# Performance work log

Measured on AMD Instinct MI355X. Metric: run time of the kernel, lower is better.

Reference implementation:

```python
import jax, jax.numpy as jnp
import numpy as np

# dims
B, L, DM, DS, K, E, DFF, R = 16, 1024, 512, 16, 4, 2, 2048, 32
DI = DM  # expand = 1 -> d_inner == d_model

PARAM_NAMES = ['m_in_w','m_conv_w','m_conv_b','m_xproj_w','m_dt_w','m_dt_b','m_A_log','m_D','m_out_w']


def setup_inputs() -> dict:
    key = jax.random.key(0)
    ks = iter(jax.random.split(key, 32))
    def rn(shape, scale=0.02):
        return jax.random.normal(next(ks), shape, dtype=jnp.float32) * scale
    inp = {
        'x': jax.random.normal(next(ks), (B, L, DM), dtype=jnp.float32),
        # per layer (E) and per direction (2: forward mamba, reversed mamba)
        'm_in_w':   rn((E, 2, 2 * DI, DM)),
        'm_conv_w': rn((E, 2, DI, K), 0.1),
        'm_conv_b': jnp.zeros((E, 2, DI), jnp.float32),
        'm_xproj_w': rn((E, 2, R + 2 * DS, DI)),
        'm_dt_w':   rn((E, 2, DI, R), 0.1),
        'm_dt_b':   jnp.full((E, 2, DI), -4.0, jnp.float32) + rn((E, 2, DI), 0.1),
        'm_A_log':  jnp.log(jnp.broadcast_to(jnp.arange(1, DS + 1, dtype=jnp.float32), (E, 2, DI, DS))),
        'm_D':      jnp.ones((E, 2, DI), jnp.float32),
        'm_out_w':  rn((E, 2, DM, DI)),
        # FFN (1x1 convs == linears) and norms per layer
        'ff_w1': rn((E, DFF, DM)), 'ff_b1': jnp.zeros((E, DFF), jnp.float32),
        'ff_w2': rn((E, DM, DFF)), 'ff_b2': jnp.zeros((E, DM), jnp.float32),
        'ln1_g': jnp.ones((E, DM), jnp.float32), 'ln1_b': jnp.zeros((E, DM), jnp.float32),
        'ln2_g': jnp.ones((E, DM), jnp.float32), 'ln2_b': jnp.zeros((E, DM), jnp.float32),
        'lnf_g': jnp.ones((DM,), jnp.float32),   'lnf_b': jnp.zeros((DM,), jnp.float32),
    }
    return inp


def layer_norm(x, g, b, eps=1e-5):
    mu = x.mean(-1, keepdims=True)
    var = ((x - mu) ** 2).mean(-1, keepdims=True)
    return (x - mu) * jax.lax.rsqrt(var + eps) * g + b


def mamba(x, in_w, conv_w, conv_b, xproj_w, dt_w, dt_b, A_log, Dp, out_w):
    # x: (B, L, DM)
    Bsz, Lseq, _ = x.shape
    xz = x @ in_w.T                       # (B, L, 2*DI)
    xc, z = jnp.split(xz, 2, axis=-1)
    # depthwise causal conv1d (kernel K, left pad K-1, truncate to L)
    xp = jnp.pad(xc, ((0, 0), (K - 1, 0), (0, 0)))
    xc = sum(conv_w[:, k] * xp[:, k:k + Lseq, :] for k in range(K)) + conv_b
    xc = jax.nn.silu(xc)
    dbl = xc @ xproj_w.T                  # (B, L, R + 2*DS)
    dt, Bm, Cm = dbl[..., :R], dbl[..., R:R + DS], dbl[..., R + DS:]
    dt = jax.nn.softplus(dt @ dt_w.T + dt_b)  # (B, L, DI)
    A = -jnp.exp(A_log)                   # (DI, DS)

    def step(h, inputs):
        dt_t, B_t, C_t, x_t = inputs      # (B,DI) (B,DS) (B,DS) (B,DI)
        dA = jnp.exp(dt_t[..., None] * A)             # (B, DI, DS)
        h = dA * h + (dt_t * x_t)[..., None] * B_t[:, None, :]
        y = jnp.einsum('bds,bs->bd', h, C_t)
        return h, y

    xs = (dt.transpose(1, 0, 2), Bm.transpose(1, 0, 2), Cm.transpose(1, 0, 2), xc.transpose(1, 0, 2))
    h0 = jnp.zeros((Bsz, DI, DS), dtype=x.dtype)
    _, ys = jax.lax.scan(step, h0, xs)    # ys: (L, B, DI)
    y = ys.transpose(1, 0, 2) + xc * Dp
    y = y * jax.nn.silu(z)
    return y @ out_w.T                    # (B, L, DM)


def _forward(x, m_in_w, m_conv_w, m_conv_b, m_xproj_w, m_dt_w, m_dt_b, m_A_log, m_D, m_out_w,
             ff_w1, ff_b1, ff_w2, ff_b2, ln1_g, ln1_b, ln2_g, ln2_b, lnf_g, lnf_b):
    packs = (m_in_w, m_conv_w, m_conv_b, m_xproj_w, m_dt_w, m_dt_b, m_A_log, m_D, m_out_w)
    for e in range(E):
        p_fwd = tuple(a[e, 0] for a in packs)
        p_rev = tuple(a[e, 1] for a in packs)
        # bidirectional mamba mixing (second block sees the time-flipped sequence)
        new_x = mamba(x, *p_fwd) + mamba(x[:, ::-1], *p_rev)[:, ::-1]
        x = x + new_x
        xn = layer_norm(x, ln1_g[e], ln1_b[e])
        y = jax.nn.gelu(xn @ ff_w1[e].T + ff_b1[e], approximate=False)
        y = y @ ff_w2[e].T + ff_b2[e]
        x = layer_norm(xn + y, ln2_g[e], ln2_b[e])
    return layer_norm(x, lnf_g, lnf_b)


def reference(x, m_in_w, m_conv_w, m_conv_b, m_xproj_w, m_dt_w, m_dt_b, m_A_log, m_D, m_out_w,
              ff_w1, ff_b1, ff_w2, ff_b2, ln1_g, ln1_b, ln2_g, ln2_b, lnf_g, lnf_b):
    return _forward(x, m_in_w, m_conv_w, m_conv_b, m_xproj_w, m_dt_w, m_dt_b, m_A_log, m_D, m_out_w,
                    ff_w1, ff_b1, ff_w2, ff_b2, ln1_g, ln1_b, ln2_g, ln2_b, lnf_g, lnf_b)
```

## Files before the change

kernel.cpp:

```cpp
#include <hip/hip_runtime.h>
#include <hip/hip_bf16.h>
#include <math.h>

#define DEVI __device__ __forceinline__

namespace {
constexpr int kL   = 1024;
constexpr int kDM  = 512;
constexpr int kDS  = 16;
constexpr int kDFF = 2048;
constexpr int kR   = 32;
constexpr int kDI  = 512;
constexpr int kB   = 16;
constexpr int kM   = kB * kL;
constexpr int kNC  = 16;
constexpr int kCH  = kL / kNC;
constexpr float kLOG2E = 1.4426950408889634f;
}

typedef __attribute__((ext_vector_type(8))) short short8;
typedef __attribute__((ext_vector_type(4))) float f32x4;

DEVI float silu_f(float x)     { return x / (1.f + __expf(-x)); }
DEVI float softplus_f(float x) { return fmaxf(x, 0.f) + log1pf(__expf(-fabsf(x))); }
DEVI float gelu_f(float x)     { return 0.5f * x * (1.f + erff(x * 0.70710678118654752f)); }

DEVI float fexp2(float x) {
    float r;
    asm("v_exp_f32 %0, %1" : "=v"(r) : "v"(x));
    return r;
}

DEVI unsigned short f2bf(float f) {
    unsigned int u = __float_as_uint(f);
    return (unsigned short)((u + 0x7fffu + ((u >> 16) & 1u)) >> 16);
}
DEVI float bf2f(unsigned short u) {
    return __uint_as_float(((unsigned int)u) << 16);
}
DEVI uint2 pack4(float4 v) {
    uint2 p;
    p.x = (unsigned int)f2bf(v.x) | ((unsigned int)f2bf(v.y) << 16);
    p.y = (unsigned int)f2bf(v.z) | ((unsigned int)f2bf(v.w) << 16);
    return p;
}

DEVI void powtree16(float r, float* qq) {
    qq[0] = r;
#pragma unroll
    for (int s = 1; s < 16; ++s) {
        int a = (s - 1) >> 1, b = (s - 1) - a;
        qq[s] = qq[a] * qq[b];
    }
}

typedef const __attribute__((address_space(1))) unsigned int* gas1;
typedef __attribute__((address_space(3))) unsigned int* las3;
DEVI void gload16(const unsigned short* g, unsigned short* l) {
    __builtin_amdgcn_global_load_lds((gas1)g, (las3)l, 16, 0, 0);
}

struct WCvtArgs { const float* src[6]; unsigned int end[6]; };

__global__ __launch_bounds__(256) void cvt_weights_k(
    WCvtArgs a, unsigned short* __restrict__ dst)
{
    unsigned int i = (blockIdx.x * 256 + threadIdx.x) * 4;
    if (i >= a.end[5]) return;
    int j = 0;
    while (i >= a.end[j]) ++j;
    unsigned int base = j ? a.end[j - 1] : 0;
    float4 v = *(const float4*)&a.src[j][i - base];
    *(uint2*)&dst[i] = pack4(v);
}

__global__ __launch_bounds__(256) void init_x_k(
    const float* __restrict__ x, float* __restrict__ xo,
    unsigned short* __restrict__ xb)
{
    size_t i = (size_t)(blockIdx.x * 256 + threadIdx.x) * 4;
    float4 v = *(const float4*)&x[i];
    *(float4*)&xo[i] = v;
    *(uint2*)&xb[i] = pack4(v);
}

template <int EPI, int BN, typename CT>
__global__ __launch_bounds__(256) void gemm_bf16(
    const unsigned short* __restrict__ A, int lda, size_t zA,
    const unsigned short* __restrict__ W, size_t zW,
    CT* __restrict__ C, int ldc, size_t zC,
    const float* __restrict__ biasb, int zBias,
    const unsigned short* __restrict__ add,
    unsigned short* __restrict__ auxb, size_t zAux, int Kd)
{
    static_assert(BN == 64 || BN == 128, "");
    constexpr int NF = BN / 32;
    __shared__ alignas(16) unsigned short As[2][128 * 32];
    __shared__ alignas(16) unsigned short Ws[2][BN * 32];

    const int z = blockIdx.z;
    A += (size_t)z * zA; W += (size_t)z * zW; C += (size_t)z * zC;
    const float* bias = biasb ? biasb + (size_t)z * zBias : nullptr;
    unsigned short* aux = auxb ? auxb + (size_t)z * zAux : nullptr;

    const int gx = gridDim.x;
    int flat = blockIdx.y * gx + blockIdx.x;
    const int total = gx * gridDim.y;
    if ((total & 7) == 0) {
        int q = total >> 3;
        flat = (flat & 7) * q + (flat >> 3);
    }
    const int bx = flat % gx;
    const int by = flat / gx;

    const int tid  = threadIdx.x;
    const int lane = tid & 63;
    const int wv   = tid >> 6;
    const int wm   = wv >> 1;
    const int wn   = wv & 1;
    const int row0 = by * 128;
    const int col0 = bx * BN;

    f32x4 acc[4][NF];
#pragma unroll
    for (int m = 0; m < 4; ++m)
#pragma unroll
        for (int n = 0; n < NF; ++n) acc[m][n] = (f32x4){0.f, 0.f, 0.f, 0.f};

    const int sr  = tid >> 2;
    const int scw = (((tid & 3) ^ ((tid >> 3) & 3)) * 8);
    const unsigned short* Ag = A + (size_t)(row0 + sr) * lda + scw;
    const unsigned short* Wg = W + (size_t)(col0 + sr) * Kd + scw;

    auto stage = [&](int buf, int k0) {
        gload16(Ag + k0, &As[buf][tid * 8]);
        gload16(Ag + (size_t)64 * lda + k0, &As[buf][2048 + tid * 8]);
        gload16(Wg + k0, &Ws[buf][tid * 8]);
        if (BN == 128)
            gload16(Wg + (size_t)64 * Kd + k0, &Ws[buf][2048 + tid * 8]);
    };

    const int nt = Kd / 32;
    stage(0, 0);
    if (nt > 1) stage(1, 32);

    const int fr  = lane & 15;
    const int sw8 = (((lane >> 4) ^ ((fr >> 1) & 3)) * 8);

    for (int t = 0; t < nt; ++t) {
        const int cur = t & 1;
        if (t + 1 < nt) {
            if constexpr (BN == 128) asm volatile("s_waitcnt vmcnt(4)" ::: "memory");
            else                     asm volatile("s_waitcnt vmcnt(3)" ::: "memory");
        } else {
            asm volatile("s_waitcnt vmcnt(0)" ::: "memory");
        }
        __builtin_amdgcn_sched_barrier(0);
        __builtin_amdgcn_s_barrier();
        __builtin_amdgcn_sched_barrier(0);

        short8 af[4], bf[NF];
#pragma unroll
        for (int m = 0; m < 4; ++m)
            af[m] = *(const short8*)&As[cur][(wm * 64 + m * 16 + fr) * 32 + sw8];
#pragma unroll
        for (int n = 0; n < NF; ++n)
            bf[n] = *(const short8*)&Ws[cur][(wn * (BN / 2) + n * 16 + fr) * 32 + sw8];
        __builtin_amdgcn_s_setprio(1);
#pragma unroll
        for (int m = 0; m < 4; ++m)
#pragma unroll
            for (int n = 0; n < NF; ++n)
                acc[m][n] = __builtin_amdgcn_mfma_f32_16x16x32_bf16(
                    af[m], bf[n], acc[m][n], 0, 0, 0);
        __builtin_amdgcn_s_setprio(0);

        __builtin_amdgcn_sched_barrier(0);
        __builtin_amdgcn_s_barrier();
        __builtin_amdgcn_sched_barrier(0);
        if (t + 2 < nt) stage(cur, (t + 2) * 32);
    }

    const int cr = (lane >> 4) * 4;
#pragma unroll
    for (int m = 0; m < 4; ++m) {
#pragma unroll
        for (int n = 0; n < NF; ++n) {
            int cn = col0 + wn * (BN / 2) + n * 16 + fr;
#pragma unroll
            for (int r = 0; r < 4; ++r) {
                int rr = row0 + wm * 64 + m * 16 + cr + r;
                size_t idx = (size_t)rr * ldc + cn;
                float v = acc[m][n][r];
                if constexpr (EPI == 0) {
                    if constexpr (__is_same(CT, unsigned short)) C[idx] = f2bf(v);
                    else C[idx] = v;
                } else if constexpr (EPI == 1) {
                    float sp = softplus_f(v + bias[cn]);
                    if constexpr (__is_same(CT, unsigned short)) C[idx] = f2bf(sp);
                    else C[idx] = sp;
                } else if constexpr (EPI == 3) {
                    C[idx] = f2bf(gelu_f(v + bias[cn]));
                } else if constexpr (EPI == 4) {
                    C[idx] = v + bias[cn] + bf2f(add[idx]);
                } else {
                    C[idx] = v;
                    if (cn < 32) aux[(size_t)rr * 32 + cn] = f2bf(v);
                }
            }
        }
    }
}

__global__ __launch_bounds__(128) void conv_silu_k(
    const unsigned short* __restrict__ xz2, unsigned short* __restrict__ xcb,
    const float* __restrict__ wb, const float* __restrict__ biasb)
{
    const int task = blockIdx.x * 128 + threadIdx.x;
    const int g   = task & 63;
    const int c   = (task >> 6) & 31;
    const int b   = (task >> 11) & 15;
    const int dir = (task >> 15) & 1;
    const int d0  = g * 8;

    const unsigned short* xzd = xz2 + (size_t)dir * 1024 + (size_t)b * kL * 2048 + d0;
    unsigned short* xc = xcb + (size_t)dir * kM * kDI + (size_t)b * kL * kDI + d0;
    const float* w    = wb + (size_t)dir * 2048;
    const float* bias = biasb + (size_t)dir * 512;

    float wk[4][8];
#pragma unroll
    for (int k = 0; k < 4; ++k)
#pragma unroll
        for (int j = 0; j < 8; ++j)
            wk[k][j] = w[(d0 + j) * 4 + (dir ? 3 - k : k)];
    float bs[8];
#pragma unroll
    for (int j = 0; j < 8; ++j) bs[j] = bias[d0 + j];

    const int t0 = c * 32;
    const int rbase = dir ? t0 : t0 - 3;

    auto loadrow = [&](int t, float* o) {
        if (t < 0 || t >= kL) {
#pragma unroll
            for (int j = 0; j < 8; ++j) o[j] = 0.f;
            return;
        }
        uint4 p = *(const uint4*)&xzd[(size_t)t * 2048];
        o[0] = bf2f((unsigned short)(p.x & 0xffff));
        o[1] = bf2f((unsigned short)(p.x >> 16));
        o[2] = bf2f((unsigned short)(p.y & 0xffff));
        o[3] = bf2f((unsigned short)(p.y >> 16));
        o[4] = bf2f((unsigned short)(p.z & 0xffff));
        o[5] = bf2f((unsigned short)(p.z >> 16));
        o[6] = bf2f((unsigned short)(p.w & 0xffff));
        o[7] = bf2f((unsigned short)(p.w >> 16));
    };

    float x0[8], x1[8], x2[8];
    loadrow(rbase + 0, x0);
    loadrow(rbase + 1, x1);
    loadrow(rbase + 2, x2);

#pragma unroll 4
    for (int i = 0; i < 32; ++i) {
        float x3[8];
        loadrow(rbase + 3 + i, x3);
        unsigned short o[8];
#pragma unroll
        for (int j = 0; j < 8; ++j) {
            float v = bs[j];
            v = fmaf(wk[0][j], x0[j], v);
            v = fmaf(wk[1][j], x1[j], v);
            v = fmaf(wk[2][j], x2[j], v);
            v = fmaf(wk[3][j], x3[j], v);
            o[j] = f2bf(silu_f(v));
        }
        *(uint4*)&xc[(size_t)(t0 + i) * kDI] = *(uint4*)o;
#pragma unroll
        for (int j = 0; j < 8; ++j) { x0[j] = x1[j]; x1[j] = x2[j]; x2[j] = x3[j]; }
    }
}

__global__ __launch_bounds__(256) void scan_chunk(
    const unsigned short* __restrict__ dtb2, const unsigned short* __restrict__ xcb2,
    const float* __restrict__ dbl2, const float* __restrict__ A_logb,
    float* __restrict__ S2, float* __restrict__ sdt2)
{
    int dir = blockIdx.y;
    const unsigned short* dtb = dtb2 + (size_t)dir * kM * kDI;
    const unsigned short* xcb = xcb2 + (size_t)dir * kM * kDI;
    const float* dbl = dbl2 + (size_t)dir * kM * 64;
    const float* A_log = A_logb + (size_t)dir * 8192;
    float* S   = S2 + (size_t)dir * (kB * kNC * kDS * kDI);
    float* sdt = sdt2 + (size_t)dir * (kB * kNC * kDI);

    int blk  = blockIdx.x;
    int dblk = blk & 1;
    int c    = (blk >> 1) & (kNC - 1);
    int b    = blk >> 5;
    int d    = dblk * 256 + threadIdx.x;

    __shared__ float blds[kCH][16];
    {
        int i = threadIdx.x >> 2, q = (threadIdx.x & 3) * 4;
        int t = dir ? (kL - 1 - (c * kCH + i)) : (c * kCH + i);
        *(float4*)&blds[i][q] =
            *(const float4*)&dbl[(size_t)(b * kL + t) * 64 + kR + q];
    }
    __syncthreads();

    const float* al = A_log + d * kDS;
    float A2[16];
#pragma unroll
    for (int s = 0; s < 16; ++s) A2[s] = -__expf(al[s]) * kLOG2E;

    bool fast = true;
#pragma unroll
    for (int s = 1; s < 16; ++s)
        fast = fast && (fabsf(A2[s] - A2[0] * (float)(s + 1)) <= 1e-4f * fabsf(A2[s]));

    float h[16];
#pragma unroll
    for (int s = 0; s < 16; ++s) h[s] = 0.f;
    float sum = 0.f;

    if (fast) {
        const float A0 = A2[0];
#pragma unroll 2
        for (int i = 0; i < kCH; ++i) {
            int p   = c * kCH + i;
            int t   = dir ? (kL - 1 - p) : p;
            int row = b * kL + t;
            float dt = bf2f(dtb[(size_t)row * kDI + d]);
            float xv = bf2f(xcb[(size_t)row * kDI + d]);
            sum += dt;
            float dx = dt * xv;
            float qq[16];
            powtree16(fexp2(dt * A0), qq);
            const float4* bp = (const float4*)&blds[i][0];
            float4 b0 = bp[0], b1 = bp[1], b2 = bp[2], b3 = bp[3];
            float Bv[16] = {b0.x, b0.y, b0.z, b0.w, b1.x, b1.y, b1.z, b1.w,
                            b2.x, b2.y, b2.z, b2.w, b3.x, b3.y, b3.z, b3.w};
#pragma unroll
            for (int s = 0; s < 16; ++s)
                h[s] = fmaf(qq[s], h[s], dx * Bv[s]);
        }
    } else {
#pragma unroll 2
        for (int i = 0; i < kCH; ++i) {
            int p   = c * kCH + i;
            int t   = dir ? (kL - 1 - p) : p;
            int row = b * kL + t;
            float dt = bf2f(dtb[(size_t)row * kDI + d]);
            float xv = bf2f(xcb[(size_t)row * kDI + d]);
            sum += dt;
            float dx = dt * xv;
            const float4* bp = (const float4*)&blds[i][0];
            float4 b0 = bp[0], b1 = bp[1], b2 = bp[2], b3 = bp[3];
            float Bv[16] = {b0.x, b0.y, b0.z, b0.w, b1.x, b1.y, b1.z, b1.w,
                            b2.x, b2.y, b2.z, b2.w, b3.x, b3.y, b3.z, b3.w};
#pragma unroll
            for (int s = 0; s < 16; ++s) {
                float q = fexp2(dt * A2[s]);
                h[s] = fmaf(q, h[s], dx * Bv[s]);
            }
        }
    }
    size_t base = (size_t)(b * kNC + c) * kDS * kDI + d;
#pragma unroll
    for (int s = 0; s < 16; ++s) S[base + s * kDI] = h[s];
    sdt[(size_t)(b * kNC + c) * kDI + d] = sum;
}

__global__ __launch_bounds__(256) void scan_carry(
    float* __restrict__ S2, const float* __restrict__ sdt2,
    const float* __restrict__ A_logb)
{
    int dir = blockIdx.y;
    float* S = S2 + (size_t)dir * (kB * kNC * kDS * kDI);
    const float* sdt = sdt2 + (size_t)dir * (kB * kNC * kDI);
    const float* A_log = A_logb + (size_t)dir * 8192;

    int g = blockIdx.x * 256 + threadIdx.x;
    int d = g & (kDI - 1);
    int s = (g >> 9) & 15;
    int b = g >> 13;

    float A2 = -__expf(A_log[d * kDS + s]) * kLOG2E;
    float h = 0.f;
#pragma unroll
    for (int c = 0; c < kNC; ++c) {
        size_t base = ((size_t)(b * kNC + c) * kDS + s) * kDI + d;
        float sv = S[base];
        float sd = sdt[(size_t)(b * kNC + c) * kDI + d];
        S[base] = h;
        h = fmaf(fexp2(sd * A2), h, sv);
    }
}

__global__ __launch_bounds__(256) void scan_emit(
    const unsigned short* __restrict__ dtb2, const unsigned short* __restrict__ xcb2,
    const float* __restrict__ dbl2, const float* __restrict__ A_logb,
    const float* __restrict__ h0v2, const float* __restrict__ Dpb,
    const unsigned short* __restrict__ xz2, unsigned short* __restrict__ yb2)
{
    int dir = blockIdx.y;
    const unsigned short* dtb = dtb2 + (size_t)dir * kM * kDI;
    const unsigned short* xcb = xcb2 + (size_t)dir * kM * kDI;
    const float* dbl = dbl2 + (size_t)dir * kM * 64;
    const float* A_log = A_logb + (size_t)dir * 8192;
    const float* h0v = h0v2 + (size_t)dir * (kB * kNC * kDS * kDI);
    const float* Dp = Dpb + (size_t)dir * 512;
    const unsigned short* zg = xz2 + (size_t)dir * 1024 + 512;
    unsigned short* yb = yb2 + (size_t)dir * kM * kDI;

    int blk  = blockIdx.x;
    int dblk = blk & 1;
    int c    = (blk >> 1) & (kNC - 1);
    int b    = blk >> 5;
    int d    = dblk * 256 + threadIdx.x;

    __shared__ float bclds[kCH][32];
    {
        int i0 = threadIdx.x >> 3, q = (threadIdx.x & 7) * 4;
#pragma unroll
        for (int rr = 0; rr < 2; ++rr) {
            int i = i0 + rr * 32;
            int t = dir ? (kL - 1 - (c * kCH + i)) : (c * kCH + i);
            *(float4*)&bclds[i][q] =
                *(const float4*)&dbl[(size_t)(b * kL + t) * 64 + kR + q];
        }
    }
    __syncthreads();

    const float* al = A_log + d * kDS;
    float A2[16];
#pragma unroll
    for (int s = 0; s < 16; ++s) A2[s] = -__expf(al[s]) * kLOG2E;
    float Dd = Dp[d];

    bool fast = true;
#pragma unroll
    for (int s = 1; s < 16; ++s)
        fast = fast && (fabsf(A2[s] - A2[0] * (float)(s + 1)) <= 1e-4f * fabsf(A2[s]));

    size_t hbase = (size_t)(b * kNC + c) * kDS * kDI + d;
    float h[16];
#pragma unroll
    for (int s = 0; s < 16; ++s) h[s] = h0v[hbase + s * kDI];

    if (fast) {
        const float A0 = A2[0];
#pragma unroll 2
        for (int i = 0; i < kCH; ++i) {
            int p   = c * kCH + i;
            int t   = dir ? (kL - 1 - p) : p;
            int row = b * kL + t;
            float dt = bf2f(dtb[(size_t)row * kDI + d]);
            float xv = bf2f(xcb[(size_t)row * kDI + d]);
            float dx = dt * xv;
            float qq[16];
            powtree16(fexp2(dt * A0), qq);
            const float4* bp = (const float4*)&bclds[i][0];
            const float4* cp = (const float4*)&bclds[i][16];
            float4 b0 = bp[0], b1 = bp[1], b2 = bp[2], b3 = bp[3];
            float4 c0 = cp[0], c1 = cp[1], c2 = cp[2], c3 = cp[3];
            float Bv[16] = {b0.x, b0.y, b0.z, b0.w, b1.x, b1.y, b1.z, b1.w,
                            b2.x, b2.y, b2.z, b2.w, b3.x, b3.y, b3.z, b3.w};
            float Cv[16] = {c0.x, c0.y, c0.z, c0.w, c1.x, c1.y, c1.z, c1.w,
                            c2.x, c2.y, c2.z, c2.w, c3.x, c3.y, c3.z, c3.w};
            float y = 0.f;
#pragma unroll
            for (int s = 0; s < 16; ++s) {
                h[s] = fmaf(qq[s], h[s], dx * Bv[s]);
                y = fmaf(h[s], Cv[s], y);
            }
            y += xv * Dd;
            float zv = bf2f(zg[(size_t)row * 2048 + d]);
            yb[(size_t)row * kDI + d] = f2bf(y * silu_f(zv));
        }
    } else {
#pragma unroll 2
        for (int i = 0; i < kCH; ++i) {
            int p   = c * kCH + i;
            int t   = dir ? (kL - 1 - p) : p;
            int row = b * kL + t;
            float dt = bf2f(dtb[(size_t)row * kDI + d]);
            float xv = bf2f(xcb[(size_t)row * kDI + d]);
            float dx = dt * xv;
            const float4* bp = (const float4*)&bclds[i][0];
            const float4* cp = (const float4*)&bclds[i][16];
            float4 b0 = bp[0], b1 = bp[1], b2 = bp[2], b3 = bp[3];
            float4 c0 = cp[0], c1 = cp[1], c2 = cp[2], c3 = cp[3];
            float Bv[16] = {b0.x, b0.y, b0.z, b0.w, b1.x, b1.y, b1.z, b1.w,
                            b2.x, b2.y, b2.z, b2.w, b3.x, b3.y, b3.z, b3.w};
            float Cv[16] = {c0.x, c0.y, c0.z, c0.w, c1.x, c1.y, c1.z, c1.w,
                            c2.x, c2.y, c2.z, c2.w, c3.x, c3.y, c3.z, c3.w};
            float y = 0.f;
#pragma unroll
            for (int s = 0; s < 16; ++s) {
                float q = fexp2(dt * A2[s]);
                h[s] = fmaf(q, h[s], dx * Bv[s]);
                y = fmaf(h[s], Cv[s], y);
            }
            y += xv * Dd;
            float zv = bf2f(zg[(size_t)row * 2048 + d]);
            yb[(size_t)row * kDI + d] = f2bf(y * silu_f(zv));
        }
    }
}

__global__ __launch_bounds__(128) void ln_k(
    const float* __restrict__ in, const unsigned short* __restrict__ a0,
    const unsigned short* __restrict__ a1,
    const float* __restrict__ g, const float* __restrict__ bb,
    float* __restrict__ out, unsigned short* __restrict__ outbf)
{
    int row = blockIdx.x;
    int tid = threadIdx.x;
    size_t off = (size_t)row * kDM + tid * 4;
    float4 v = *(const float4*)&in[off];
    if (a0) {
        uint2 u0 = *(const uint2*)&a0[off];
        uint2 u1 = *(const uint2*)&a1[off];
        v.x += bf2f((unsigned short)(u0.x & 0xffff)) + bf2f((unsigned short)(u1.x & 0xffff));
        v.y += bf2f((unsigned short)(u0.x >> 16))    + bf2f((unsigned short)(u1.x >> 16));
        v.z += bf2f((unsigned short)(u0.y & 0xffff)) + bf2f((unsigned short)(u1.y & 0xffff));
        v.w += bf2f((unsigned short)(u0.y >> 16))    + bf2f((unsigned short)(u1.y >> 16));
    }
    float s1 = v.x + v.y + v.z + v.w;
    float s2 = v.x * v.x + v.y * v.y + v.z * v.z + v.w * v.w;
#pragma unroll
    for (int o = 32; o >= 1; o >>= 1) {
        s1 += __shfl_xor(s1, o);
        s2 += __shfl_xor(s2, o);
    }
    __shared__ float red[4];
    if ((tid & 63) == 0) { red[(tid >> 6) * 2] = s1; red[(tid >> 6) * 2 + 1] = s2; }
    __syncthreads();
    s1 = red[0] + red[2];
    s2 = red[1] + red[3];
    float mu  = s1 * (1.f / kDM);
    float var = s2 * (1.f / kDM) - mu * mu;
    float rs  = rsqrtf(var + 1e-5f);
    int cn = tid * 4;
    float4 gv = *(const float4*)&g[cn];
    float4 bv = *(const float4*)&bb[cn];
    float4 o;
    o.x = (v.x - mu) * rs * gv.x + bv.x;
    o.y = (v.y - mu) * rs * gv.y + bv.y;
    o.z = (v.z - mu) * rs * gv.z + bv.z;
    o.w = (v.w - mu) * rs * gv.w + bv.w;
    if (out)
        *(float4*)&out[off] = o;
    if (outbf)
        *(uint2*)&outbf[off] = pack4(o);
}

extern "C" void kernel_launch(void* const* d_in, const int* in_sizes, int n_in,
                              void* d_out, int out_size, void* d_ws, size_t ws_size,
                              hipStream_t stream)
{
    const float* x_in    = (const float*)d_in[0];
    const float* in_w    = (const float*)d_in[1];
    const float* conv_w  = (const float*)d_in[2];
    const float* conv_b  = (const float*)d_in[3];
    const float* xproj_w = (const float*)d_in[4];
    const float* dt_w    = (const float*)d_in[5];
    const float* dt_b    = (const float*)d_in[6];
    const float* A_log   = (const float*)d_in[7];
    const float* Dp      = (const float*)d_in[8];
    const float* out_w   = (const float*)d_in[9];
    const float* ff_w1   = (const float*)d_in[10];
    const float* ff_b1   = (const float*)d_in[11];
    const float* ff_w2   = (const float*)d_in[12];
    const float* ff_b2   = (const float*)d_in[13];
    const float* ln1_g   = (const float*)d_in[14];
    const float* ln1_b   = (const float*)d_in[15];
    const float* ln2_g   = (const float*)d_in[16];
    const float* ln2_b   = (const float*)d_in[17];
    const float* lnf_g   = (const float*)d_in[18];
    const float* lnf_b   = (const float*)d_in[19];

    float* ws = (float*)d_ws;
    unsigned short* wsb = (unsigned short*)d_ws;

    unsigned short* wb_in  = wsb;
    unsigned short* wb_xp  = wsb + 2097152;
    unsigned short* wb_out = wsb + 2228224;
    unsigned short* wb_f1  = wsb + 3276800;
    unsigned short* wb_f2  = wsb + 5373952;
    unsigned short* wb_dt  = wsb + 7471104;

    constexpr size_t A0 = 3768320;
    unsigned short* xbf  = (unsigned short*)(ws + A0);
    unsigned short* xz2  = (unsigned short*)(ws + A0 + 4194304);
    unsigned short* xcb2 = (unsigned short*)(ws + A0 + 20971520);
    unsigned short* yb2  = (unsigned short*)(ws + A0 + 29360128);
    float*          Sb2  = ws + A0 + 37748736;
    unsigned short* dtb2 = (unsigned short*)(ws + A0 + 46137344);
    float*          dbl2 = ws + A0 + 54525952;
    unsigned short* dtin2= (unsigned short*)(ws + A0 + 56623104);
    float*          sdt2 = ws + A0 + 57147392;
    unsigned short* o2   = (unsigned short*)(ws + A0 + 37748736);
    unsigned short* xnbf = (unsigned short*)(ws + A0 + 8388608);
    unsigned short* Hb   = (unsigned short*)(ws + A0 + 12582912);
    float*          t2   = ws + A0 + 29360128;

    float* xcur = (float*)d_out;
    dim3 thr(256);

    WCvtArgs wa;
    wa.src[0] = in_w;    wa.end[0] = 2097152;
    wa.src[1] = xproj_w; wa.end[1] = 2228224;
    wa.src[2] = out_w;   wa.end[2] = 3276800;
    wa.src[3] = ff_w1;   wa.end[3] = 5373952;
    wa.src[4] = ff_w2;   wa.end[4] = 7471104;
    wa.src[5] = dt_w;    wa.end[5] = 7536640;
    cvt_weights_k<<<dim3(7536640 / 1024), thr, 0, stream>>>(wa, wsb);
    init_x_k<<<dim3(8192), thr, 0, stream>>>(x_in, xcur, xbf);

    for (int e = 0; e < 2; ++e) {
        gemm_bf16<0, 128, unsigned short><<<dim3(16, 128), thr, 0, stream>>>(
            xbf, 512, 0, wb_in + (size_t)e * 1048576, 0, xz2, 2048, 0,
            nullptr, 0, nullptr, nullptr, 0, 512);
        conv_silu_k<<<dim3(512), dim3(128), 0, stream>>>(
            xz2, xcb2, conv_w + (size_t)e * 4096, conv_b + (size_t)e * 1024);
        gemm_bf16<5, 64, float><<<dim3(1, 128, 2), thr, 0, stream>>>(
            xcb2, 512, (size_t)kM * 512, wb_xp + (size_t)e * 65536, 32768,
            dbl2, 64, (size_t)kM * 64, nullptr, 0, nullptr,
            dtin2, (size_t)kM * 32, 512);
        gemm_bf16<1, 128, unsigned short><<<dim3(4, 128, 2), thr, 0, stream>>>(
            dtin2, 32, (size_t)kM * 32, wb_dt + (size_t)e * 32768, 16384,
            dtb2, 512, (size_t)kM * 512, dt_b + (size_t)e * 1024, 512,
            nullptr, nullptr, 0, 32);
        scan_chunk<<<dim3(kB * kNC * 2, 2), thr, 0, stream>>>(
            dtb2, xcb2, dbl2, A_log + (size_t)e * 16384, Sb2, sdt2);
        scan_carry<<<dim3(512, 2), thr, 0, stream>>>(
            Sb2, sdt2, A_log + (size_t)e * 16384);
        scan_emit<<<dim3(kB * kNC * 2, 2), thr, 0, stream>>>(
            dtb2, xcb2, dbl2, A_log + (size_t)e * 16384, Sb2,
            Dp + (size_t)e * 1024, xz2, yb2);
        gemm_bf16<0, 128, unsigned short><<<dim3(4, 128, 2), thr, 0, stream>>>(
            yb2, 512, (size_t)kM * 512, wb_out + (size_t)e * 524288, 262144,
            o2, 512, (size_t)kM * 512, nullptr, 0, nullptr, nullptr, 0, 512);
        ln_k<<<dim3(kM), dim3(128), 0, stream>>>(
            xcur, o2, o2 + (size_t)kM * 512,
            ln1_g + e * kDM, ln1_b + e * kDM, nullptr, xnbf);
        gemm_bf16<3, 128, unsigned short><<<dim3(16, 128), thr, 0, stream>>>(
            xnbf, 512, 0, wb_f1 + (size_t)e * 1048576, 0, Hb, 2048, 0,
            ff_b1 + (size_t)e * kDFF, 0, nullptr, nullptr, 0, 512);
        gemm_bf16<4, 128, float><<<dim3(4, 128), thr, 0, stream>>>(
            Hb, 2048, 0, wb_f2 + (size_t)e * 1048576, 0, t2, 512, 0,
            ff_b2 + (size_t)e * kDM, 0, xnbf, nullptr, 0, 2048);
        ln_k<<<dim3(kM), dim3(128), 0, stream>>>(
            t2, nullptr, nullptr, ln2_g + e * kDM, ln2_b + e * kDM, xcur,
            e == 0 ? xbf : nullptr);
    }
    ln_k<<<dim3(kM), dim3(128), 0, stream>>>(
        xcur, nullptr, nullptr, lnf_g, lnf_b, xcur, nullptr);
}
```

Measured before the change: 853.6 us.

## Fold dt projection into x_proj GEMM via precomputed combined weight

Precomputes W_dtc = dt_w @ xproj_w[:32] so that dt = xc @ W_dtc^T comes out of the same GEMM as the B/C projection, in a new epilogue mode that applies softplus and writes bf16 dt. This removes the separate low-rank dt GEMM and the round trip of the rank-32 intermediate through memory. The cost is a full 512x512 K=512 GEMM per direction in place of the rank-32 pair, so more FLOPs, plus a small weight-build kernel per call. It also changes rounding, since the combined weight is stored in bf16.

```diff
diff --git a/kernel.cpp b/kernel.cpp
--- a/kernel.cpp
+++ b/kernel.cpp
@@ -74,6 +74,23 @@
     *(uint2*)&dst[i] = pack4(v);
 }
 
+__global__ __launch_bounds__(256) void build_dtc_k(
+    const float* __restrict__ xproj_w, const float* __restrict__ dt_w,
+    unsigned short* __restrict__ out)
+{
+    int z = blockIdx.z;
+    const float* xp = xproj_w + (size_t)z * 32768;
+    const float* dw = dt_w + (size_t)z * 16384;
+    unsigned short* o = out + (size_t)z * 262144;
+    int idx = blockIdx.x * 256 + threadIdx.x;
+    int j = idx >> 9, k = idx & 511;
+    float acc = 0.f;
+#pragma unroll
+    for (int r = 0; r < 32; ++r)
+        acc = fmaf(dw[j * 32 + r], xp[r * 512 + k], acc);
+    o[idx] = f2bf(acc);
+}
+
 __global__ __launch_bounds__(256) void init_x_k(
     const float* __restrict__ x, float* __restrict__ xo,
     unsigned short* __restrict__ xb)
@@ -88,6 +105,7 @@
 __global__ __launch_bounds__(256) void gemm_bf16(
     const unsigned short* __restrict__ A, int lda, size_t zA,
     const unsigned short* __restrict__ W, size_t zW,
+    const unsigned short* __restrict__ Wdb, size_t zWd,
     CT* __restrict__ C, int ldc, size_t zC,
     const float* __restrict__ biasb, int zBias,
     const unsigned short* __restrict__ add,
@@ -130,7 +148,14 @@
     const int sr  = tid >> 2;
     const int scw = (((tid & 3) ^ ((tid >> 3) & 3)) * 8);
     const unsigned short* Ag = A + (size_t)(row0 + sr) * lda + scw;
-    const unsigned short* Wg = W + (size_t)(col0 + sr) * Kd + scw;
+    const unsigned short* Wg;
+    if constexpr (EPI == 6) {
+        const unsigned short* Wsel = (bx == 0) ? W : (Wdb + (size_t)z * zWd);
+        int wr = (bx == 0) ? col0 : (col0 - 64);
+        Wg = Wsel + (size_t)(wr + sr) * Kd + scw;
+    } else {
+        Wg = W + (size_t)(col0 + sr) * Kd + scw;
+    }
 
     auto stage = [&](int buf, int k0) {
         gload16(Ag + k0, &As[buf][tid * 8]);
@@ -195,17 +220,17 @@
                 if constexpr (EPI == 0) {
                     if constexpr (__is_same(CT, unsigned short)) C[idx] = f2bf(v);
                     else C[idx] = v;
-                } else if constexpr (EPI == 1) {
-                    float sp = softplus_f(v + bias[cn]);
-                    if constexpr (__is_same(CT, unsigned short)) C[idx] = f2bf(sp);
-                    else C[idx] = sp;
                 } else if constexpr (EPI == 3) {
                     C[idx] = f2bf(gelu_f(v + bias[cn]));
                 } else if constexpr (EPI == 4) {
                     C[idx] = v + bias[cn] + bf2f(add[idx]);
                 } else {
-                    C[idx] = v;
-                    if (cn < 32) aux[(size_t)rr * 32 + cn] = f2bf(v);
+                    if (cn < 64) {
+                        C[(size_t)rr * 64 + cn] = v;
+                    } else {
+                        aux[(size_t)rr * 512 + (cn - 64)] =
+                            f2bf(softplus_f(v + bias[cn - 64]));
+                    }
                 }
             }
         }
@@ -602,7 +627,7 @@
     float*          Sb2  = ws + A0 + 37748736;
     unsigned short* dtb2 = (unsigned short*)(ws + A0 + 46137344);
     float*          dbl2 = ws + A0 + 54525952;
-    unsigned short* dtin2= (unsigned short*)(ws + A0 + 56623104);
+    unsigned short* wb_dtc = (unsigned short*)(ws + A0 + 56623104);
     float*          sdt2 = ws + A0 + 57147392;
     unsigned short* o2   = (unsigned short*)(ws + A0 + 37748736);
     unsigned short* xnbf = (unsigned short*)(ws + A0 + 8388608);
@@ -620,22 +645,22 @@
     wa.src[4] = ff_w2;   wa.end[4] = 7471104;
     wa.src[5] = dt_w;    wa.end[5] = 7536640;
     cvt_weights_k<<<dim3(7536640 / 1024), thr, 0, stream>>>(wa, wsb);
+    build_dtc_k<<<dim3(1024, 1, 4), thr, 0, stream>>>(xproj_w, dt_w, wb_dtc);
     init_x_k<<<dim3(8192), thr, 0, stream>>>(x_in, xcur, xbf);
 
     for (int e = 0; e < 2; ++e) {
         gemm_bf16<0, 128, unsigned short><<<dim3(16, 128), thr, 0, stream>>>(
-            xbf, 512, 0, wb_in + (size_t)e * 1048576, 0, xz2, 2048, 0,
-            nullptr, 0, nullptr, nullptr, 0, 512);
+            xbf, 512, 0, wb_in + (size_t)e * 1048576, 0, nullptr, 0,
+            xz2, 2048, 0, nullptr, 0, nullptr, nullptr, 0, 512);
         conv_silu_k<<<dim3(512), dim3(128), 0, stream>>>(
             xz2, xcb2, conv_w + (size_t)e * 4096, conv_b + (size_t)e * 1024);
-        gemm_bf16<5, 64, float><<<dim3(1, 128, 2), thr, 0, stream>>>(
-            xcb2, 512, (size_t)kM * 512, wb_xp + (size_t)e * 65536, 32768,
-            dbl2, 64, (size_t)kM * 64, nullptr, 0, nullptr,
-            dtin2, (size_t)kM * 32, 512);
-        gemm_bf16<1, 128, unsigned short><<<dim3(4, 128, 2), thr, 0, stream>>>(
-            dtin2, 32, (size_t)kM * 32, wb_dt + (size_t)e * 32768, 16384,
-            dtb2, 512, (size_t)kM * 512, dt_b + (size_t)e * 1024, 512,
-            nullptr, nullptr, 0, 32);
+        gemm_bf16<6, 64, float><<<dim3(9, 128, 2), thr, 0, stream>>>(
+            xcb2, 512, (size_t)kM * 512,
+            wb_xp + (size_t)e * 65536, 32768,
+            wb_dtc + (size_t)e * 524288, 262144,
+            dbl2, 64, (size_t)kM * 64,
+            dt_b + (size_t)e * 1024, 512,
+            nullptr, dtb2, (size_t)kM * 512, 512);
         scan_chunk<<<dim3(kB * kNC * 2, 2), thr, 0, stream>>>(
             dtb2, xcb2, dbl2, A_log + (size_t)e * 16384, Sb2, sdt2);
         scan_carry<<<dim3(512, 2), thr, 0, stream>>>(
@@ -645,16 +670,19 @@
             Dp + (size_t)e * 1024, xz2, yb2);
         gemm_bf16<0, 128, unsigned short><<<dim3(4, 128, 2), thr, 0, stream>>>(
             yb2, 512, (size_t)kM * 512, wb_out + (size_t)e * 524288, 262144,
-            o2, 512, (size_t)kM * 512, nullptr, 0, nullptr, nullptr, 0, 512);
+            nullptr, 0, o2, 512, (size_t)kM * 512, nullptr, 0,
+            nullptr, nullptr, 0, 512);
         ln_k<<<dim3(kM), dim3(128), 0, stream>>>(
             xcur, o2, o2 + (size_t)kM * 512,
             ln1_g + e * kDM, ln1_b + e * kDM, nullptr, xnbf);
         gemm_bf16<3, 128, unsigned short><<<dim3(16, 128), thr, 0, stream>>>(
-            xnbf, 512, 0, wb_f1 + (size_t)e * 1048576, 0, Hb, 2048, 0,
-            ff_b1 + (size_t)e * kDFF, 0, nullptr, nullptr, 0, 512);
+            xnbf, 512, 0, wb_f1 + (size_t)e * 1048576, 0, nullptr, 0,
+            Hb, 2048, 0, ff_b1 + (size_t)e * kDFF, 0, nullptr,
+            nullptr, 0, 512);
         gemm_bf16<4, 128, float><<<dim3(4, 128), thr, 0, stream>>>(
-            Hb, 2048, 0, wb_f2 + (size_t)e * 1048576, 0, t2, 512, 0,
-            ff_b2 + (size_t)e * kDM, 0, xnbf, nullptr, 0, 2048);
+            Hb, 2048, 0, wb_f2 + (size_t)e * 1048576, 0, nullptr, 0,
+            t2, 512, 0, ff_b2 + (size_t)e * kDM, 0, xnbf,
+            nullptr, 0, 2048);
         ln_k<<<dim3(kM), dim3(128), 0, stream>>>(
             t2, nullptr, nullptr, ln2_g + e * kDM, ln2_b + e * kDM, xcur,
             e == 0 ? xbf : nullptr);
```

Result: slower. 911.3 us (+6.8%).
